# Performance work log

Measured on AMD Instinct MI355X. Metric: run time of the kernel, lower is better.

## Reference

```python
import jax, jax.numpy as jnp
import numpy as np

B, T, C, A, P = 16, 1024, 512, 4096, 256  # batch, frames, phones, allophone arcs, phonemes


def setup_inputs() -> dict:
    key = jax.random.key(0)
    k1, k2, k3 = jax.random.split(key, 3)
    hs_pad = jax.random.normal(k1, (B, T, C), dtype=jnp.float32)
    # each phone has exactly A // C allophone arcs (full coverage, balanced)
    phone_arc_labels = jnp.arange(A, dtype=jnp.int32) % C
    arcs_per_phone = A // C
    # weights near -log(arcs_per_phone) so sum_a exp(log_prob + w) ~= 1,
    # matching a trained allophone layer and keeping the redis step log-safe
    alloW = 0.01 * jax.random.normal(k2, (A,), dtype=jnp.float32) - jnp.log(
        jnp.float32(arcs_per_phone)
    )
    phoneme_arc_labels = jax.random.randint(k3, (A,), 0, P, dtype=jnp.int32)
    return {
        "hs_pad": hs_pad,
        "alloW": alloW,
        "phone_arc_labels": phone_arc_labels,
        "phoneme_arc_labels": phoneme_arc_labels,
        "n_phonemes": P,
    }


def reference(hs_pad, alloW, phone_arc_labels, phoneme_arc_labels, n_phonemes):
    # log_softmax over phones
    log_probs = jax.nn.log_softmax(hs_pad, axis=-1)  # [B,T,C]
    # WFST intersection of linear emission graph with 1-state allophone graph:
    # arc a gets weight log_probs[..., phone_label(a)] + alloW[a]
    new_emissions = log_probs[..., phone_arc_labels] + alloW  # [B,T,A]
    # squash many phones per phoneme: exp + scatter-add over output labels
    ex = jnp.exp(new_emissions)
    Bq, Tq = ex.shape[0], ex.shape[1]
    squashed = jnp.zeros((Bq, Tq, n_phonemes), dtype=ex.dtype)
    squashed = squashed.at[..., phoneme_arc_labels].add(ex)  # [B,T,P]
    # redistribute probability mass so it sums to 1
    redistributed = (squashed.sum(axis=-1) - 1.0)[..., None] / n_phonemes
    squashed = squashed - redistributed
    return jnp.log(squashed)
```

## Files before the change

kernel.cpp:

```cpp
#include <hip/hip_runtime.h>
#include <hip/hip_bf16.h>

#define BT   16384
#define CDIM 512
#define ADIM 4096
#define PDIM 256

typedef __attribute__((ext_vector_type(8))) short  short8;
typedef __attribute__((ext_vector_type(8))) unsigned short ushort8;
typedef __attribute__((ext_vector_type(4))) float  f32x4;

__device__ __forceinline__ unsigned short bf16_rne(float f) {
    unsigned int u = __float_as_uint(f);
    u += 0x7FFFu + ((u >> 16) & 1u);
    return (unsigned short)(u >> 16);
}

__global__ __launch_bounds__(256) void build_Wf(const float* __restrict__ alloW,
                                                const int* __restrict__ phone_lab,
                                                const int* __restrict__ phoneme_lab,
                                                unsigned short* __restrict__ Wf) {
    __shared__ float wrow[32 * PDIM];
    const int bx = blockIdx.x;
    const int t  = threadIdx.x;

#pragma unroll
    for (int i = 0; i < 32; ++i) wrow[i * 256 + t] = 0.0f;
    __syncthreads();

#pragma unroll
    for (int i = 0; i < ADIM / 256; ++i) {
        int a = i * 256 + t;
        int c = phone_lab[a];
        if ((c >> 5) == bx)
            atomicAdd(&wrow[(c & 31) * 256 + phoneme_lab[a]], __expf(alloW[a]));
    }
    __syncthreads();

    ushort8 pk[4];
#pragma unroll
    for (int g = 0; g < 4; ++g) {
#pragma unroll
        for (int j = 0; j < 8; ++j)
            pk[g][j] = bf16_rne(wrow[(g * 8 + j) * 256 + t]);
    }
    unsigned short* dst = Wf + (size_t)bx * (PDIM * 32) + t * 32;
#pragma unroll
    for (int g = 0; g < 4; ++g)
        *(ushort8*)(dst + g * 8) = pk[g];
}

__global__ __launch_bounds__(512, 2) void allo_fused(const float* __restrict__ hs,
                                                     const unsigned short* __restrict__ Wf,
                                                     float* __restrict__ out) {
    __shared__ __align__(16) unsigned short Af[4 * 16 * 16 * 32];
    __shared__ float invZ[64];
    __shared__ float psum[4][64];

    const int tid  = threadIdx.x;
    const int wave = tid >> 6;
    const int lane = tid & 63;
    const int row0 = blockIdx.x * 64;

    {
        const int r    = tid >> 3;
        const int ksl  = tid & 7;
        const int rblk = r >> 4;
        const int cc   = r & 15;
        const float* hsr = hs + (size_t)(row0 + r) * CDIM + ksl * 4;
        unsigned short* af = Af + rblk * 8192 + cc * 32 + ksl * 4;

        float s = 0.0f;
#pragma unroll
        for (int h = 0; h < 2; ++h) {
            float4 v[8];
#pragma unroll
            for (int i = 0; i < 8; ++i)
                v[i] = *(const float4*)(hsr + (h * 8 + i) * 32);
#pragma unroll
            for (int i = 0; i < 8; ++i) {
                float e0 = __expf(v[i].x), e1 = __expf(v[i].y);
                float e2 = __expf(v[i].z), e3 = __expf(v[i].w);
                s += (e0 + e1) + (e2 + e3);
                ushort4 pk;
                pk.x = bf16_rne(e0); pk.y = bf16_rne(e1);
                pk.z = bf16_rne(e2); pk.w = bf16_rne(e3);
                *(ushort4*)(af + (h * 8 + i) * 512) = pk;
            }
        }
        s += __shfl_xor(s, 1);
        s += __shfl_xor(s, 2);
        s += __shfl_xor(s, 4);
        if (ksl == 0) invZ[r] = 1.0f / s;
    }
    __syncthreads();

    const int c        = lane & 15;
    const int q        = lane >> 4;
    const int rowhalf  = wave >> 2;
    const int cg       = wave & 3;

    f32x4 acc[2][4];
#pragma unroll
    for (int rb = 0; rb < 2; ++rb)
#pragma unroll
        for (int cb = 0; cb < 4; ++cb)
            acc[rb][cb] = (f32x4){0.f, 0.f, 0.f, 0.f};

    const unsigned short* wb  = Wf + (size_t)(cg * 64 + c) * 32 + q * 8;
    const unsigned short* af0 = Af + (size_t)rowhalf * 16384 + c * 32 + q * 8;

#pragma unroll 4
    for (int kb = 0; kb < 16; ++kb) {
        short8 a0 = *(const short8*)(af0 + kb * 512);
        short8 a1 = *(const short8*)(af0 + 8192 + kb * 512);

        const unsigned short* wkb = wb + (size_t)kb * 8192;
        short8 b0 = *(const short8*)(wkb);
        short8 b1 = *(const short8*)(wkb + 512);
        short8 b2 = *(const short8*)(wkb + 1024);
        short8 b3 = *(const short8*)(wkb + 1536);

        acc[0][0] = __builtin_amdgcn_mfma_f32_16x16x32_bf16(a0, b0, acc[0][0], 0, 0, 0);
        acc[0][1] = __builtin_amdgcn_mfma_f32_16x16x32_bf16(a0, b1, acc[0][1], 0, 0, 0);
        acc[0][2] = __builtin_amdgcn_mfma_f32_16x16x32_bf16(a0, b2, acc[0][2], 0, 0, 0);
        acc[0][3] = __builtin_amdgcn_mfma_f32_16x16x32_bf16(a0, b3, acc[0][3], 0, 0, 0);
        acc[1][0] = __builtin_amdgcn_mfma_f32_16x16x32_bf16(a1, b0, acc[1][0], 0, 0, 0);
        acc[1][1] = __builtin_amdgcn_mfma_f32_16x16x32_bf16(a1, b1, acc[1][1], 0, 0, 0);
        acc[1][2] = __builtin_amdgcn_mfma_f32_16x16x32_bf16(a1, b2, acc[1][2], 0, 0, 0);
        acc[1][3] = __builtin_amdgcn_mfma_f32_16x16x32_bf16(a1, b3, acc[1][3], 0, 0, 0);
    }

    float sv[2][4];
#pragma unroll
    for (int rb = 0; rb < 2; ++rb)
#pragma unroll
        for (int r = 0; r < 4; ++r) {
            float x = (acc[rb][0][r] + acc[rb][1][r]) + (acc[rb][2][r] + acc[rb][3][r]);
            x += __shfl_xor(x, 1);
            x += __shfl_xor(x, 2);
            x += __shfl_xor(x, 4);
            x += __shfl_xor(x, 8);
            sv[rb][r] = x;
        }
    if (c == 0) {
#pragma unroll
        for (int rb = 0; rb < 2; ++rb)
#pragma unroll
            for (int r = 0; r < 4; ++r)
                psum[cg][rowhalf * 32 + rb * 16 + q * 4 + r] = sv[rb][r];
    }
    __syncthreads();

#pragma unroll
    for (int rb = 0; rb < 2; ++rb)
#pragma unroll
        for (int r = 0; r < 4; ++r) {
            const int rr = rowhalf * 32 + rb * 16 + q * 4 + r;
            const float iz = invZ[rr];
            const float S  = ((psum[0][rr] + psum[1][rr]) + (psum[2][rr] + psum[3][rr])) * iz;
            const float corr = (S - 1.0f) * (1.0f / (float)PDIM);
            float* orow = out + (size_t)(row0 + rr) * PDIM + cg * 64 + c;
#pragma unroll
            for (int cb = 0; cb < 4; ++cb)
                orow[cb * 16] = __logf(acc[rb][cb][r] * iz - corr);
        }
}

extern "C" void kernel_launch(void* const* d_in, const int* in_sizes, int n_in,
                              void* d_out, int out_size, void* d_ws, size_t ws_size,
                              hipStream_t stream) {
    const float* hs          = (const float*)d_in[0];
    const float* alloW       = (const float*)d_in[1];
    const int*   phone_lab   = (const int*)d_in[2];
    const int*   phoneme_lab = (const int*)d_in[3];
    float*       out         = (float*)d_out;

    unsigned short* Wf = (unsigned short*)d_ws;

    build_Wf<<<CDIM / 32, 256, 0, stream>>>(alloW, phone_lab, phoneme_lab, Wf);
    allo_fused<<<BT / 64, 512, 0, stream>>>(hs, Wf, out);
}
```

Baseline: 100.1 us.

## Precompute per-phone weight row sums to drop cross-wave reduction; halve rows per block

After: 99.70 us. About the same (-0.4%).

```diff
diff --git a/kernel.cpp b/kernel.cpp
--- a/kernel.cpp
+++ b/kernel.cpp
@@ -19,7 +19,8 @@
 __global__ __launch_bounds__(256) void build_Wf(const float* __restrict__ alloW,
                                                 const int* __restrict__ phone_lab,
                                                 const int* __restrict__ phoneme_lab,
-                                                unsigned short* __restrict__ Wf) {
+                                                unsigned short* __restrict__ Wf,
+                                                float* __restrict__ rowsumW) {
     __shared__ float wrow[32 * PDIM];
     const int bx = blockIdx.x;
     const int t  = threadIdx.x;
@@ -48,57 +49,76 @@
 #pragma unroll
     for (int g = 0; g < 4; ++g)
         *(ushort8*)(dst + g * 8) = pk[g];
+
+    {
+        const int i = t >> 3, j = t & 7;
+        float s = 0.0f;
+#pragma unroll
+        for (int m = 0; m < 32; ++m) s += wrow[i * 256 + j * 32 + m];
+        s += __shfl_xor(s, 1);
+        s += __shfl_xor(s, 2);
+        s += __shfl_xor(s, 4);
+        if (j == 0) rowsumW[bx * 32 + i] = s;
+    }
 }
 
-__global__ __launch_bounds__(512, 2) void allo_fused(const float* __restrict__ hs,
+__global__ __launch_bounds__(256, 2) void allo_fused(const float* __restrict__ hs,
                                                      const unsigned short* __restrict__ Wf,
+                                                     const float* __restrict__ rowsumW,
                                                      float* __restrict__ out) {
-    __shared__ __align__(16) unsigned short Af[4 * 16 * 16 * 32];
-    __shared__ float invZ[64];
-    __shared__ float psum[4][64];
+    __shared__ __align__(16) unsigned short Af[2 * 16 * 16 * 32];
+    __shared__ float invZ[32];
+    __shared__ float corrS[32];
 
     const int tid  = threadIdx.x;
     const int wave = tid >> 6;
     const int lane = tid & 63;
-    const int row0 = blockIdx.x * 64;
+    const int row0 = blockIdx.x * 32;
 
     {
-        const int r    = tid >> 3;
-        const int ksl  = tid & 7;
-        const int rblk = r >> 4;
-        const int cc   = r & 15;
+        const int r   = tid >> 3;
+        const int ksl = tid & 7;
+        const int rb  = r >> 4;
+        const int cc  = r & 15;
         const float* hsr = hs + (size_t)(row0 + r) * CDIM + ksl * 4;
-        unsigned short* af = Af + rblk * 8192 + cc * 32 + ksl * 4;
+        const float* rsw = rowsumW + ksl * 4;
+        unsigned short* af = Af + rb * 8192 + cc * 32 + ksl * 4;
 
-        float s = 0.0f;
+        float s = 0.0f, sw = 0.0f;
 #pragma unroll
         for (int h = 0; h < 2; ++h) {
-            float4 v[8];
+            float4 v[8], w[8];
 #pragma unroll
-            for (int i = 0; i < 8; ++i)
+            for (int i = 0; i < 8; ++i) {
                 v[i] = *(const float4*)(hsr + (h * 8 + i) * 32);
+                w[i] = *(const float4*)(rsw + (h * 8 + i) * 32);
+            }
 #pragma unroll
             for (int i = 0; i < 8; ++i) {
                 float e0 = __expf(v[i].x), e1 = __expf(v[i].y);
                 float e2 = __expf(v[i].z), e3 = __expf(v[i].w);
                 s += (e0 + e1) + (e2 + e3);
+                sw = fmaf(e0, w[i].x, sw); sw = fmaf(e1, w[i].y, sw);
+                sw = fmaf(e2, w[i].z, sw); sw = fmaf(e3, w[i].w, sw);
                 ushort4 pk;
                 pk.x = bf16_rne(e0); pk.y = bf16_rne(e1);
                 pk.z = bf16_rne(e2); pk.w = bf16_rne(e3);
                 *(ushort4*)(af + (h * 8 + i) * 512) = pk;
             }
         }
-        s += __shfl_xor(s, 1);
-        s += __shfl_xor(s, 2);
-        s += __shfl_xor(s, 4);
-        if (ksl == 0) invZ[r] = 1.0f / s;
+        s  += __shfl_xor(s, 1);  sw += __shfl_xor(sw, 1);
+        s  += __shfl_xor(s, 2);  sw += __shfl_xor(sw, 2);
+        s  += __shfl_xor(s, 4);  sw += __shfl_xor(sw, 4);
+        if (ksl == 0) {
+            const float iz = 1.0f / s;
+            invZ[r]  = iz;
+            corrS[r] = (sw * iz - 1.0f) * (1.0f / (float)PDIM);
+        }
     }
     __syncthreads();
 
-    const int c        = lane & 15;
-    const int q        = lane >> 4;
-    const int rowhalf  = wave >> 2;
-    const int cg       = wave & 3;
+    const int c = lane & 15;
+    const int q = lane >> 4;
 
     f32x4 acc[2][4];
 #pragma unroll
@@ -107,8 +127,8 @@
         for (int cb = 0; cb < 4; ++cb)
             acc[rb][cb] = (f32x4){0.f, 0.f, 0.f, 0.f};
 
-    const unsigned short* wb  = Wf + (size_t)(cg * 64 + c) * 32 + q * 8;
-    const unsigned short* af0 = Af + (size_t)rowhalf * 16384 + c * 32 + q * 8;
+    const unsigned short* wb  = Wf + (size_t)(wave * 64 + c) * 32 + q * 8;
+    const unsigned short* af0 = Af + c * 32 + q * 8;
 
 #pragma unroll 4
     for (int kb = 0; kb < 16; ++kb) {
@@ -131,39 +151,17 @@
         acc[1][3] = __builtin_amdgcn_mfma_f32_16x16x32_bf16(a1, b3, acc[1][3], 0, 0, 0);
     }
 
-    float sv[2][4];
 #pragma unroll
     for (int rb = 0; rb < 2; ++rb)
 #pragma unroll
         for (int r = 0; r < 4; ++r) {
-            float x = (acc[rb][0][r] + acc[rb][1][r]) + (acc[rb][2][r] + acc[rb][3][r]);
-            x += __shfl_xor(x, 1);
-            x += __shfl_xor(x, 2);
-            x += __shfl_xor(x, 4);
-            x += __shfl_xor(x, 8);
-            sv[rb][r] = x;
-        }
-    if (c == 0) {
-#pragma unroll
-        for (int rb = 0; rb < 2; ++rb)
-#pragma unroll
-            for (int r = 0; r < 4; ++r)
-                psum[cg][rowhalf * 32 + rb * 16 + q * 4 + r] = sv[rb][r];
-    }
-    __syncthreads();
-
-#pragma unroll
-    for (int rb = 0; rb < 2; ++rb)
-#pragma unroll
-        for (int r = 0; r < 4; ++r) {
-            const int rr = rowhalf * 32 + rb * 16 + q * 4 + r;
+            const int rr = rb * 16 + q * 4 + r;
             const float iz = invZ[rr];
-            const float S  = ((psum[0][rr] + psum[1][rr]) + (psum[2][rr] + psum[3][rr])) * iz;
-            const float corr = (S - 1.0f) * (1.0f / (float)PDIM);
-            float* orow = out + (size_t)(row0 + rr) * PDIM + cg * 64 + c;
+            const float co = corrS[rr];
+            float* orow = out + (size_t)(row0 + rr) * PDIM + wave * 64 + c;
 #pragma unroll
             for (int cb = 0; cb < 4; ++cb)
-                orow[cb * 16] = __logf(acc[rb][cb][r] * iz - corr);
+                orow[cb * 16] = __logf(acc[rb][cb][r] * iz - co);
         }
 }
 
@@ -176,8 +174,9 @@
     const int*   phoneme_lab = (const int*)d_in[3];
     float*       out         = (float*)d_out;
 
-    unsigned short* Wf = (unsigned short*)d_ws;
+    unsigned short* Wf      = (unsigned short*)d_ws;
+    float*          rowsumW = (float*)((char*)d_ws + (256 << 10));
 
-    build_Wf<<<CDIM / 32, 256, 0, stream>>>(alloW, phone_lab, phoneme_lab, Wf);
-    allo_fused<<<BT / 64, 512, 0, stream>>>(hs, Wf, out);
+    build_Wf<<<CDIM / 32, 256, 0, stream>>>(alloW, phone_lab, phoneme_lab, Wf, rowsumW);
+    allo_fused<<<BT / 32, 256, 0, stream>>>(hs, Wf, rowsumW, out);
 }
```
